# Kernel tuning notes

Hardware: AMD Instinct MI355X
Metric: run time of the kernel (lower is better)

## Reference

```python
import jax, jax.numpy as jnp
import numpy as np

D = 256
K = 64


def setup_inputs() -> dict:
    key = jax.random.key(0)
    k1, k2, k3 = jax.random.split(key, 3)
    B, H, W = 16, 96, 96
    X = jax.random.normal(k1, (B, D, H, W), dtype=jnp.float32)
    std1 = 1.0 / float(np.sqrt(K * D))
    std2 = 1.0 / float(np.sqrt(K))
    codewords = jax.random.uniform(k2, (K, D), dtype=jnp.float32, minval=-std1, maxval=std1)
    scale = jax.random.uniform(k3, (K,), dtype=jnp.float32, minval=-std2, maxval=std2)
    return {"X": X, "codewords": codewords, "scale": scale}


def reference(X, codewords, scale):
    # X: [B, D, H, W] -> Xf: [B, N, D]
    B = X.shape[0]
    Xf = X.reshape(B, X.shape[1], -1).transpose(0, 2, 1)
    # Scaled L2 distances: SL[b,n,k] = scale[k] * ||x_bn - c_k||^2
    x2 = jnp.sum(Xf * Xf, axis=-1, keepdims=True)          # [B, N, 1]
    c2 = jnp.sum(codewords * codewords, axis=-1)            # [K]
    xc = jnp.einsum('bnd,kd->bnk', Xf, codewords)           # [B, N, K]
    SL = scale * (x2 - 2.0 * xc + c2)                       # [B, N, K]
    # Assignment weights: softmax over codewords K
    A = jax.nn.softmax(SL, axis=-1)                         # [B, N, K]
    # Aggregate residuals: E[b,k,d] = sum_n A[b,n,k] * (X[b,n,d] - C[k,d])
    E = jnp.einsum('bnk,bnd->bkd', A, Xf) - jnp.sum(A, axis=1)[:, :, None] * codewords
    return E
```

## Files before the change

### kernel.cpp

```cpp
#include <hip/hip_runtime.h>

#define NDIM  256
#define NK    64
#define NPIX  9216
#define NB    16
#define TN    64
#define NW    32
#define GRID  (NB*NW)

typedef _Float16 half2_t __attribute__((ext_vector_type(2)));
typedef _Float16 half4_t __attribute__((ext_vector_type(4)));
typedef _Float16 half8_t __attribute__((ext_vector_type(8)));
typedef float    f32x4  __attribute__((ext_vector_type(4)));

__device__ __forceinline__ float fdot2(half2_t a, half2_t b, float c) {
  return __builtin_amdgcn_fdot2(a, b, c, false);
}

#define BAR() asm volatile("s_waitcnt lgkmcnt(0)\n\ts_barrier" ::: "memory")

#define OFF_ASUM   0
#define OFF_APART  (NB * NK)
#define OFF_EPART  (OFF_APART + GRID * NK)
#define WS_NEED    ((size_t)OFF_EPART * 4 + (size_t)GRID * NK * NDIM * 2)

__global__ __launch_bounds__(256, 2) void encode_main(
    const float* __restrict__ X, const float* __restrict__ Cw,
    const float* __restrict__ scale,
    void* __restrict__ Eout, float* __restrict__ Aout, int mode)
{
  __shared__ _Float16 XbS[2][32 * 66 * 8];
  __shared__ _Float16 Al[NK][72];
  __shared__ float red2[4][TN];
  __shared__ float redM[4][TN];
  __shared__ float redS[4][TN];

  const int tid  = threadIdx.x;
  const int w    = __builtin_amdgcn_readfirstlane(tid >> 6);
  const int lane = tid & 63;
  const int m    = lane & 15, quad = lane >> 4;
  const int b    = blockIdx.x & 15;
  const int wid  = blockIdx.x >> 4;
  const int ntiles = (wid < 16) ? 5 : 4;
  const int pix0   = (wid * 4 + (wid < 16 ? wid : 16)) * TN;
  const float* Xbase = X + (size_t)b * NDIM * NPIX;
  const int kbase = w * 16;

  float xv[64];
  {
    const float* Xg = Xbase + (size_t)(w * 64) * NPIX + pix0 + lane;
#pragma unroll
    for (int i = 0; i < 64; ++i) xv[i] = Xg[(size_t)i * NPIX];
  }

  {
    const int kk = tid >> 2, ch = tid & 3;
    const float* Cr = Cw + kk * NDIM + ch * 64;
    float s = 0.f;
#pragma unroll
    for (int j = 0; j < 16; ++j) {
      const float4 v = *(const float4*)(Cr + 4 * j);
      s += v.x * v.x + v.y * v.y + v.z * v.z + v.w * v.w;
    }
    redM[ch][kk] = s;
  }

  half8_t af1[8];
#pragma unroll
  for (int ks = 0; ks < 8; ++ks) {
    const float* ap = Cw + (kbase + m) * NDIM + ks * 32 + quad * 8;
    const float4 a0 = *(const float4*)(ap);
    const float4 a1 = *(const float4*)(ap + 4);
    half8_t h;
    h[0] = (_Float16)a0.x; h[1] = (_Float16)a0.y;
    h[2] = (_Float16)a0.z; h[3] = (_Float16)a0.w;
    h[4] = (_Float16)a1.x; h[5] = (_Float16)a1.y;
    h[6] = (_Float16)a1.z; h[7] = (_Float16)a1.w;
    af1[ks] = h;
    __builtin_amdgcn_sched_barrier(0);
  }

  const float4 scv = *(const float4*)(scale + kbase + quad * 4);
  const float sc[4] = {scv.x, scv.y, scv.z, scv.w};

  BAR();
  float sq[4];
#pragma unroll
  for (int r = 0; r < 4; ++r) {
    const int k = kbase + quad * 4 + r;
    const float c2k = redM[0][k] + redM[1][k] + redM[2][k] + redM[3][k];
    sq[r] = sc[r] * c2k;
  }

  f32x4 acc_e[4][4];
#pragma unroll
  for (int i = 0; i < 4; ++i)
#pragma unroll
    for (int j = 0; j < 4; ++j)
      acc_e[i][j] = (f32x4){0.f, 0.f, 0.f, 0.f};
  float asum_acc = 0.f;

  auto STAGE = [&](int bufi) {
    _Float16* Xb = XbS[bufi];
    float xsq = 0.f;
#pragma unroll
    for (int g = 0; g < 8; ++g) {
      half8_t hv;
#pragma unroll
      for (int i = 0; i < 8; ++i) {
        const float v = xv[g * 8 + i];
        hv[i] = (_Float16)v; xsq += v * v;
      }
      *(half8_t*)&Xb[((w * 8 + g) * 66 + lane) * 8] = hv;
    }
    red2[w][lane] = xsq;
  };
  auto ISSUE = [&](int t) {
    const float* Xg = Xbase + (size_t)(w * 64) * NPIX + pix0 + t * TN + lane;
#pragma unroll
    for (int i = 0; i < 64; ++i) xv[i] = Xg[(size_t)i * NPIX];
  };

  STAGE(0);
  ISSUE(1);
  BAR();

  for (int tt = 0; tt < ntiles; ++tt) {
    const _Float16* Xb = XbS[tt & 1];

    f32x4 accs[4];
#pragma unroll
    for (int nt = 0; nt < 4; ++nt) accs[nt] = (f32x4){0.f, 0.f, 0.f, 0.f};
    __builtin_amdgcn_s_setprio(1);
#pragma unroll
    for (int ks = 0; ks < 8; ++ks) {
#pragma unroll
      for (int nt = 0; nt < 4; ++nt) {
        const half8_t bf = *(const half8_t*)&Xb[((ks * 4 + quad) * 66 + nt * 16 + m) * 8];
        accs[nt] = __builtin_amdgcn_mfma_f32_16x16x32_f16(af1[ks], bf, accs[nt], 0, 0, 0);
      }
    }
    __builtin_amdgcn_s_setprio(0);

    float e[4][4], mw[4];
#pragma unroll
    for (int nt = 0; nt < 4; ++nt) {
      const int p = nt * 16 + m;
      const float x2p = red2[0][p] + red2[1][p] + red2[2][p] + red2[3][p];
      float L[4];
      float mx = -3.0e38f;
#pragma unroll
      for (int r = 0; r < 4; ++r) {
        L[r] = sc[r] * x2p - 2.f * sc[r] * accs[nt][r] + sq[r];
        mx = fmaxf(mx, L[r]);
      }
      mx = fmaxf(mx, __shfl_xor(mx, 16));
      mx = fmaxf(mx, __shfl_xor(mx, 32));
      float s = 0.f;
#pragma unroll
      for (int r = 0; r < 4; ++r) { e[nt][r] = __expf(L[r] - mx); s += e[nt][r]; }
      s += __shfl_xor(s, 16);
      s += __shfl_xor(s, 32);
      mw[nt] = mx;
      if (lane < 16) { redM[w][p] = mx; redS[w][p] = s; }
    }
    BAR();
#pragma unroll
    for (int nt = 0; nt < 4; ++nt) {
      const int p = nt * 16 + m;
      const float M = fmaxf(fmaxf(redM[0][p], redM[1][p]),
                            fmaxf(redM[2][p], redM[3][p]));
      const float T = redS[0][p] * __expf(redM[0][p] - M)
                    + redS[1][p] * __expf(redM[1][p] - M)
                    + redS[2][p] * __expf(redM[2][p] - M)
                    + redS[3][p] * __expf(redM[3][p] - M);
      const float norm = __expf(mw[nt] - M) / T;
#pragma unroll
      for (int r = 0; r < 4; ++r)
        Al[kbase + quad * 4 + r][p] = (_Float16)(e[nt][r] * norm);
    }
    BAR();

    __builtin_amdgcn_s_setprio(1);
#pragma unroll
    for (int ks = 0; ks < 2; ++ks) {
      half8_t ba[4];
#pragma unroll
      for (int kt = 0; kt < 4; ++kt)
        ba[kt] = *(const half8_t*)&Al[kt * 16 + m][ks * 32 + quad * 8];
#pragma unroll
      for (int dt = 0; dt < 4; ++dt) {
        const int c = w * 8 + dt * 2 + (m >> 3);
        const int dlow = m & 7;
        half8_t xa;
#pragma unroll
        for (int j = 0; j < 8; ++j)
          xa[j] = Xb[(c * 66 + ks * 32 + quad * 8 + j) * 8 + dlow];
#pragma unroll
        for (int kt = 0; kt < 4; ++kt)
          acc_e[dt][kt] = __builtin_amdgcn_mfma_f32_16x16x32_f16(xa, ba[kt], acc_e[dt][kt], 0, 0, 0);
      }
    }
    __builtin_amdgcn_s_setprio(0);

    {
      const half2_t one = {(_Float16)1.f, (_Float16)1.f};
      const int ka = kbase + (lane >> 2);
      const int pa = (lane & 3) * 16;
      float s = 0.f;
#pragma unroll
      for (int lc = 0; lc < 2; ++lc) {
        const half8_t sv = *(const half8_t*)&Al[ka][pa + lc * 8];
        s = fdot2(__builtin_shufflevector(sv, sv, 0, 1), one, s);
        s = fdot2(__builtin_shufflevector(sv, sv, 2, 3), one, s);
        s = fdot2(__builtin_shufflevector(sv, sv, 4, 5), one, s);
        s = fdot2(__builtin_shufflevector(sv, sv, 6, 7), one, s);
      }
      s += __shfl_xor(s, 1);
      s += __shfl_xor(s, 2);
      asum_acc += s;
    }

    if (tt + 1 < ntiles) {
      STAGE((tt + 1) & 1);
      if (tt + 2 < ntiles) ISSUE(tt + 2);
      BAR();
    }
  }

  BAR();
  _Float16* Et = XbS[0];
#pragma unroll
  for (int dt = 0; dt < 4; ++dt)
#pragma unroll
    for (int kt = 0; kt < 4; ++kt)
#pragma unroll
      for (int r = 0; r < 4; ++r) {
        const int k = kt * 16 + m;
        const int d = w * 64 + dt * 16 + quad * 4 + r;
        Et[k * 264 + d] = (_Float16)acc_e[dt][kt][r];
      }
  BAR();
  const int ko = tid >> 2, cq = tid & 3;
  if (mode) {
    _Float16* Ebk = (_Float16*)Eout + (size_t)blockIdx.x * (NK * NDIM);
#pragma unroll
    for (int g = 0; g < 8; ++g)
      *(half8_t*)&Ebk[ko * NDIM + cq * 64 + g * 8] =
          *(const half8_t*)&Et[ko * 264 + cq * 64 + g * 8];
    if ((lane & 3) == 0)
      Aout[blockIdx.x * NK + kbase + (lane >> 2)] = asum_acc;
  } else {
    float* Ebk = (float*)Eout + (size_t)b * (NK * NDIM);
#pragma unroll
    for (int g = 0; g < 64; ++g)
      atomicAdd(&Ebk[ko * NDIM + cq * 64 + g], (float)Et[ko * 264 + cq * 64 + g]);
    if ((lane & 3) == 0)
      atomicAdd(&Aout[b * NK + kbase + (lane >> 2)], asum_acc);
  }
}

__global__ void finalize_partials(const _Float16* __restrict__ EpartH,
                                  const float* __restrict__ Apart,
                                  const float* __restrict__ Cw,
                                  float* __restrict__ out) {
  const int g = blockIdx.x * 256 + threadIdx.x;
  const int i0 = g * 4;
  const int bb = i0 >> 14;
  const int o  = i0 & 16383;
  const int k  = o >> 8, d = i0 & 255;
  float a = 0.f;
#pragma unroll 8
  for (int w = 0; w < NW; ++w) a += Apart[(w * NB + bb) * NK + k];
  float s0 = 0.f, s1 = 0.f, s2 = 0.f, s3 = 0.f;
  const _Float16* base = EpartH + o;
#pragma unroll 4
  for (int w = 0; w < NW; ++w) {
    const half4_t v = *(const half4_t*)(base + (((size_t)(w * NB + bb)) << 14));
    s0 += (float)v[0]; s1 += (float)v[1];
    s2 += (float)v[2]; s3 += (float)v[3];
  }
  const float4 c0 = *(const float4*)(Cw + k * NDIM + d);
  float4 r0;
  r0.x = s0 - a * c0.x; r0.y = s1 - a * c0.y;
  r0.z = s2 - a * c0.z; r0.w = s3 - a * c0.w;
  *(float4*)(out + i0) = r0;
}

__global__ void finalize_atomic(const float* __restrict__ E_acc,
                                const float* __restrict__ asum,
                                const float* __restrict__ Cw,
                                float* __restrict__ out) {
  const int i = blockIdx.x * 256 + threadIdx.x;
  const int d = i & 255;
  const int k = (i >> 8) & 63;
  const int bb = i >> 14;
  out[i] = E_acc[i] - asum[bb * NK + k] * Cw[k * NDIM + d];
}

extern "C" void kernel_launch(void* const* d_in, const int* in_sizes, int n_in,
                              void* d_out, int out_size, void* d_ws, size_t ws_size,
                              hipStream_t stream) {
  const float* X     = (const float*)d_in[0];
  const float* Cw    = (const float*)d_in[1];
  const float* scale = (const float*)d_in[2];
  float* out = (float*)d_out;

  float* wsf = (float*)d_ws;
  float* asum  = wsf + OFF_ASUM;
  float* Apart = wsf + OFF_APART;

  if (ws_size >= WS_NEED) {
    _Float16* EpartH = (_Float16*)(wsf + OFF_EPART);
    encode_main<<<GRID, 256, 0, stream>>>(X, Cw, scale, EpartH, Apart, 1);
    finalize_partials<<<(NB*NK*NDIM)/(256*4), 256, 0, stream>>>(EpartH, Apart, Cw, out);
  } else {
    float* E_acc = wsf + OFF_APART;
    hipMemsetAsync(wsf, 0,
                   (size_t)(NB*NK + NB*NK*NDIM) * sizeof(float), stream);
    encode_main<<<GRID, 256, 0, stream>>>(X, Cw, scale, E_acc, asum, 0);
    finalize_atomic<<<(NB*NK*NDIM)/256, 256, 0, stream>>>(E_acc, asum, Cw, out);
  }
}
```

Measured before the change: 236.5 us.

## Stage X tile as fp32 with float4 loads and swizzled single-buffer LDS

Replaces the double-buffered fp16 LDS staging of the X tile with a single fp32 LDS buffer filled by float4 global loads and an XOR swizzle to avoid bank conflicts. Conversion to fp16 moves into the MFMA operand loads, and the squared-norm reduction now uses shuffles. The aim is wider, more coalesced global loads and a cheaper conversion path. In exchange it drops the double buffering, adds an extra barrier per tile, doubles LDS traffic for the first GEMM, and needs gathered strided LDS reads for the B operand, which may lower occupancy since the fp32 buffer is larger.

```diff
diff --git a/kernel.cpp b/kernel.cpp
--- a/kernel.cpp
+++ b/kernel.cpp
@@ -29,7 +29,7 @@
     const float* __restrict__ scale,
     void* __restrict__ Eout, float* __restrict__ Aout, int mode)
 {
-  __shared__ _Float16 XbS[2][32 * 66 * 8];
+  __shared__ float XbF[256 * 64];
   __shared__ _Float16 Al[NK][72];
   __shared__ float red2[4][TN];
   __shared__ float redM[4][TN];
@@ -39,6 +39,7 @@
   const int w    = __builtin_amdgcn_readfirstlane(tid >> 6);
   const int lane = tid & 63;
   const int m    = lane & 15, quad = lane >> 4;
+  const int q0   = lane >> 4, x15 = lane & 15;
   const int b    = blockIdx.x & 15;
   const int wid  = blockIdx.x >> 4;
   const int ntiles = (wid < 16) ? 5 : 4;
@@ -46,12 +47,15 @@
   const float* Xbase = X + (size_t)b * NDIM * NPIX;
   const int kbase = w * 16;
 
-  float xv[64];
-  {
-    const float* Xg = Xbase + (size_t)(w * 64) * NPIX + pix0 + lane;
-#pragma unroll
-    for (int i = 0; i < 64; ++i) xv[i] = Xg[(size_t)i * NPIX];
-  }
+  float4 xv4[16];
+  auto ISSUE = [&](int t) {
+    const float* Xg = Xbase + (size_t)(w * 64 + q0) * NPIX
+                            + pix0 + t * TN + 4 * x15;
+#pragma unroll
+    for (int i = 0; i < 16; ++i)
+      xv4[i] = *(const float4*)(Xg + (size_t)(4 * i) * NPIX);
+  };
+  ISSUE(0);
 
   {
     const int kk = tid >> 2, ch = tid & 3;
@@ -100,33 +104,32 @@
       acc_e[i][j] = (f32x4){0.f, 0.f, 0.f, 0.f};
   float asum_acc = 0.f;
 
-  auto STAGE = [&](int bufi) {
-    _Float16* Xb = XbS[bufi];
-    float xsq = 0.f;
-#pragma unroll
-    for (int g = 0; g < 8; ++g) {
-      half8_t hv;
-#pragma unroll
-      for (int i = 0; i < 8; ++i) {
-        const float v = xv[g * 8 + i];
-        hv[i] = (_Float16)v; xsq += v * v;
-      }
-      *(half8_t*)&Xb[((w * 8 + g) * 66 + lane) * 8] = hv;
-    }
-    red2[w][lane] = xsq;
-  };
-  auto ISSUE = [&](int t) {
-    const float* Xg = Xbase + (size_t)(w * 64) * NPIX + pix0 + t * TN + lane;
-#pragma unroll
-    for (int i = 0; i < 64; ++i) xv[i] = Xg[(size_t)i * NPIX];
-  };
-
-  STAGE(0);
-  ISSUE(1);
-  BAR();
-
   for (int tt = 0; tt < ntiles; ++tt) {
-    const _Float16* Xb = XbS[tt & 1];
+    BAR();
+
+    {
+      float xs0 = 0.f, xs1 = 0.f, xs2 = 0.f, xs3 = 0.f;
+#pragma unroll
+      for (int i = 0; i < 16; ++i) {
+        const int d = w * 64 + 4 * i + q0;
+        const float4 v = xv4[i];
+        xs0 += v.x * v.x; xs1 += v.y * v.y;
+        xs2 += v.z * v.z; xs3 += v.w * v.w;
+        const int psw = (4 * x15) ^ (((d >> 3) & 1) << 4);
+        *(float4*)&XbF[d * 64 + psw] = v;
+      }
+      xs0 += __shfl_xor(xs0, 16); xs0 += __shfl_xor(xs0, 32);
+      xs1 += __shfl_xor(xs1, 16); xs1 += __shfl_xor(xs1, 32);
+      xs2 += __shfl_xor(xs2, 16); xs2 += __shfl_xor(xs2, 32);
+      xs3 += __shfl_xor(xs3, 16); xs3 += __shfl_xor(xs3, 32);
+      if (lane < 16) {
+        float4 t4; t4.x = xs0; t4.y = xs1; t4.z = xs2; t4.w = xs3;
+        *(float4*)&red2[w][4 * lane] = t4;
+      }
+    }
+    BAR();
+
+    if (tt + 1 < ntiles) ISSUE(tt + 1);
 
     f32x4 accs[4];
 #pragma unroll
@@ -136,7 +139,11 @@
     for (int ks = 0; ks < 8; ++ks) {
 #pragma unroll
       for (int nt = 0; nt < 4; ++nt) {
-        const half8_t bf = *(const half8_t*)&Xb[((ks * 4 + quad) * 66 + nt * 16 + m) * 8];
+        const int pxs = (nt * 16 + m) ^ ((quad & 1) << 4);
+        const float* col = &XbF[(ks * 32 + quad * 8) * 64 + pxs];
+        half8_t bf;
+#pragma unroll
+        for (int j = 0; j < 8; ++j) bf[j] = (_Float16)col[j * 64];
         accs[nt] = __builtin_amdgcn_mfma_f32_16x16x32_f16(af1[ks], bf, accs[nt], 0, 0, 0);
       }
     }
@@ -190,12 +197,15 @@
         ba[kt] = *(const half8_t*)&Al[kt * 16 + m][ks * 32 + quad * 8];
 #pragma unroll
       for (int dt = 0; dt < 4; ++dt) {
-        const int c = w * 8 + dt * 2 + (m >> 3);
-        const int dlow = m & 7;
+        const int d  = w * 64 + dt * 16 + m;
+        const int cb = ks * 32 + ((quad ^ (((m >> 3) & 1) << 1)) << 3);
+        const float4 a0 = *(const float4*)&XbF[d * 64 + cb];
+        const float4 a1 = *(const float4*)&XbF[d * 64 + cb + 4];
         half8_t xa;
-#pragma unroll
-        for (int j = 0; j < 8; ++j)
-          xa[j] = Xb[(c * 66 + ks * 32 + quad * 8 + j) * 8 + dlow];
+        xa[0] = (_Float16)a0.x; xa[1] = (_Float16)a0.y;
+        xa[2] = (_Float16)a0.z; xa[3] = (_Float16)a0.w;
+        xa[4] = (_Float16)a1.x; xa[5] = (_Float16)a1.y;
+        xa[6] = (_Float16)a1.z; xa[7] = (_Float16)a1.w;
 #pragma unroll
         for (int kt = 0; kt < 4; ++kt)
           acc_e[dt][kt] = __builtin_amdgcn_mfma_f32_16x16x32_f16(xa, ba[kt], acc_e[dt][kt], 0, 0, 0);
@@ -220,16 +230,10 @@
       s += __shfl_xor(s, 2);
       asum_acc += s;
     }
-
-    if (tt + 1 < ntiles) {
-      STAGE((tt + 1) & 1);
-      if (tt + 2 < ntiles) ISSUE(tt + 2);
-      BAR();
-    }
   }
 
   BAR();
-  _Float16* Et = XbS[0];
+  _Float16* Et = (_Float16*)XbF;
 #pragma unroll
   for (int dt = 0; dt < 4; ++dt)
 #pragma unroll
```

New measurement: 243.5 us. 1.03x slower.

## Repartition E accumulation by codeword slice per wave to drop a barrier

Applied to the files above, without the earlier changes.

Each wave now accumulates E for its own 16-codeword slice across all 256 feature dims (16 MFMA tiles), instead of a 64-dim slice across all 64 codewords. Because a wave only reads the assignment rows it wrote itself, the barrier between writing the softmax weights to LDS and the MFMA accumulation is removed. The trade-off is that every wave now reads the whole staged X tile from LDS with scalar half loads, roughly four times more X reads per wave, while the A-operand reads drop.

```diff
diff --git a/kernel.cpp b/kernel.cpp
--- a/kernel.cpp
+++ b/kernel.cpp
@@ -92,12 +92,9 @@
     sq[r] = sc[r] * c2k;
   }
 
-  f32x4 acc_e[4][4];
-#pragma unroll
-  for (int i = 0; i < 4; ++i)
-#pragma unroll
-    for (int j = 0; j < 4; ++j)
-      acc_e[i][j] = (f32x4){0.f, 0.f, 0.f, 0.f};
+  f32x4 acc_e[16];
+#pragma unroll
+  for (int i = 0; i < 16; ++i) acc_e[i] = (f32x4){0.f, 0.f, 0.f, 0.f};
   float asum_acc = 0.f;
 
   auto STAGE = [&](int bufi) {
@@ -179,26 +176,20 @@
       for (int r = 0; r < 4; ++r)
         Al[kbase + quad * 4 + r][p] = (_Float16)(e[nt][r] * norm);
     }
-    BAR();
 
     __builtin_amdgcn_s_setprio(1);
 #pragma unroll
     for (int ks = 0; ks < 2; ++ks) {
-      half8_t ba[4];
-#pragma unroll
-      for (int kt = 0; kt < 4; ++kt)
-        ba[kt] = *(const half8_t*)&Al[kt * 16 + m][ks * 32 + quad * 8];
-#pragma unroll
-      for (int dt = 0; dt < 4; ++dt) {
-        const int c = w * 8 + dt * 2 + (m >> 3);
+      const half8_t ba = *(const half8_t*)&Al[kbase + m][ks * 32 + quad * 8];
+#pragma unroll
+      for (int dtile = 0; dtile < 16; ++dtile) {
+        const int c = dtile * 2 + (m >> 3);
         const int dlow = m & 7;
         half8_t xa;
 #pragma unroll
         for (int j = 0; j < 8; ++j)
           xa[j] = Xb[(c * 66 + ks * 32 + quad * 8 + j) * 8 + dlow];
-#pragma unroll
-        for (int kt = 0; kt < 4; ++kt)
-          acc_e[dt][kt] = __builtin_amdgcn_mfma_f32_16x16x32_f16(xa, ba[kt], acc_e[dt][kt], 0, 0, 0);
+        acc_e[dtile] = __builtin_amdgcn_mfma_f32_16x16x32_f16(xa, ba, acc_e[dtile], 0, 0, 0);
       }
     }
     __builtin_amdgcn_s_setprio(0);
@@ -230,16 +221,16 @@
 
   BAR();
   _Float16* Et = XbS[0];
-#pragma unroll
-  for (int dt = 0; dt < 4; ++dt)
-#pragma unroll
-    for (int kt = 0; kt < 4; ++kt)
+  {
+    const int k = kbase + m;
+#pragma unroll
+    for (int dtile = 0; dtile < 16; ++dtile)
 #pragma unroll
       for (int r = 0; r < 4; ++r) {
-        const int k = kt * 16 + m;
-        const int d = w * 64 + dt * 16 + quad * 4 + r;
-        Et[k * 264 + d] = (_Float16)acc_e[dt][kt][r];
-      }
+        const int d = dtile * 16 + quad * 4 + r;
+        Et[k * 264 + d] = (_Float16)acc_e[dtile][r];
+      }
+  }
   BAR();
   const int ko = tid >> 2, cq = tid & 3;
   if (mode) {
```

After: 245.3 us. 1.04x slower.
